# Kernel optimization log

Hardware: AMD Instinct MI355X
Metric: run time of the kernel (lower is better)

## Reference

```python
import jax, jax.numpy as jnp
import numpy as np

EPS = 1e-8

def _cos_loss(a, b):
    # faithful to torch cos_loss: norm = sqrt(sum(x*x)), x / (norm + 1e-8)
    a_norm = jnp.sqrt(jnp.sum(a * a, axis=1, keepdims=True))
    b_norm = jnp.sqrt(jnp.sum(b * b, axis=1, keepdims=True))
    a_n = a / (a_norm + EPS)
    b_n = b / (b_norm + EPS)
    cossim = jnp.sum(a_n * b_n, axis=1)
    return jnp.mean(1.0 - cossim)

def setup_inputs() -> dict:
    key = jax.random.key(0)
    k1, k2, k3 = jax.random.split(key, 3)
    shape = (1, 768, 64, 64)  # [n, c_cat(block2 VGG16 feats), h, w]
    a = jax.random.normal(k1, shape, dtype=jnp.float32)
    b = jax.random.normal(k2, shape, dtype=jnp.float32)
    d = jax.random.normal(k3, shape, dtype=jnp.float32)
    return {"a": a, "b": b, "d": d}

def reference(a, b, d):
    n, c, h, w = a.shape
    hw = h * w
    a_flat = a.reshape(n, c, hw)   # [n, c, hw]
    b_flat = b.reshape(n, c, hw)   # [n, c, h2w2]
    d_flat = d.reshape(n, c, hw)
    # normalize exactly as argmin_cos_distance: sqrt(sum + 1e-8) then /(norm + 1e-8)
    b_norm = jnp.sqrt(jnp.sum(b_flat * b_flat, axis=1, keepdims=True) + EPS)
    b_n = b_flat / (b_norm + EPS)
    a_norm = jnp.sqrt(jnp.sum(a_flat * a_flat, axis=1, keepdims=True) + EPS)
    a_n = a_flat / (a_norm + EPS)
    # cosine distance matrix [n, hw, h2w2]
    d_mat = 1.0 - jnp.einsum('ncp,ncq->npq', a_n, b_n)
    z_best = jnp.argmin(d_mat, axis=2)  # [n, hw]
    # gather matched style features from d
    idx = jnp.broadcast_to(z_best[:, None, :], (n, c, hw))
    target_feats = jnp.take_along_axis(d_flat, idx, axis=2)  # [n, c, hw]
    # NNFM loss between rendered feats and matched style feats (score is detached)
    loss = _cos_loss(a_flat, target_feats)
    z_new = target_feats.reshape(n, c, h, w)
    return (loss, z_new, z_best)
```

## Files before the change

### kernel.cpp

```cpp
#include <hip/hip_runtime.h>
#include <math.h>

#define EPS  1e-8f
#define C    768
#define HW   4096
#define NKB  24
#define NNB  12
#define NBN  32
#define TAU  0.016f
#define NCH_NEW 12
#define NCH_OLD 48

typedef float  floatx4 __attribute__((ext_vector_type(4)));
typedef short  shortx8 __attribute__((ext_vector_type(8)));
typedef unsigned short ushort_t;
typedef unsigned int   uint_t;
typedef __attribute__((address_space(1))) uint_t as1_uint;
typedef __attribute__((address_space(3))) uint_t as3_uint;

__device__ __forceinline__ ushort_t f2bf(float v) {
    uint_t u = __float_as_uint(v);
    uint_t r = (u + 0x7FFFu + ((u >> 16) & 1u)) >> 16;
    return (ushort_t)r;
}
__device__ __forceinline__ void async_cp16(const ushort_t* g, ushort_t* l) {
    __builtin_amdgcn_global_load_lds((const as1_uint*)g, (as3_uint*)l, 16, 0, 0);
}

__global__ __launch_bounds__(256) void prep_kernel(
    const float* __restrict__ a, const float* __restrict__ b,
    const float* __restrict__ d,
    ushort_t* __restrict__ Ah, ushort_t* __restrict__ Bh,
    float* __restrict__ dT, float* __restrict__ bT,
    float* __restrict__ aT, int at_ok,
    float* __restrict__ nbp2, float* __restrict__ out)
{
    __shared__ float tile[64][65];
    const int t = threadIdx.x;
    const int p0 = blockIdx.x * 64;
    const int c0 = blockIdx.y * 64;
    const int r16 = t >> 4;
    const int q4  = (t & 15) * 4;
    const int pl = t >> 2, g = t & 3;
    const int pg = p0 + pl;
    const int sw = (pg >> 1) & 3;

    if (blockIdx.x == 0 && blockIdx.y == 0 && t == 0) out[0] = 0.f;

#pragma unroll
    for (int pp = 0; pp < 4; ++pp) {
        int c = pp * 16 + r16;
        float4 v = *(const float4*)&d[(size_t)(c0 + c) * HW + p0 + q4];
        tile[c][q4]     = v.x; tile[c][q4 + 1] = v.y;
        tile[c][q4 + 2] = v.z; tile[c][q4 + 3] = v.w;
    }
    __syncthreads();
#pragma unroll
    for (int pp = 0; pp < 4; ++pp) {
        int p = pp * 16 + r16;
        float4 v;
        v.x = tile[q4][p];     v.y = tile[q4 + 1][p];
        v.z = tile[q4 + 2][p]; v.w = tile[q4 + 3][p];
        *(float4*)&dT[(size_t)(p0 + p) * C + c0 + q4] = v;
    }
    __syncthreads();

#pragma unroll
    for (int pp = 0; pp < 4; ++pp) {
        int c = pp * 16 + r16;
        float4 v = *(const float4*)&b[(size_t)(c0 + c) * HW + p0 + q4];
        tile[c][q4]     = v.x; tile[c][q4 + 1] = v.y;
        tile[c][q4 + 2] = v.z; tile[c][q4 + 3] = v.w;
    }
    __syncthreads();
#pragma unroll
    for (int pp = 0; pp < 4; ++pp) {
        int p = pp * 16 + r16;
        float4 v;
        v.x = tile[q4][p];     v.y = tile[q4 + 1][p];
        v.z = tile[q4 + 2][p]; v.w = tile[q4 + 3][p];
        *(float4*)&bT[(size_t)(p0 + p) * C + c0 + q4] = v;
    }
#pragma unroll
    for (int h = 0; h < 2; ++h) {
        const int kb = (c0 >> 5) + h;
        uint_t w[4];
#pragma unroll
        for (int u = 0; u < 4; ++u) {
            ushort_t lo = f2bf(tile[h * 32 + g * 8 + 2 * u][pl]);
            ushort_t hi = f2bf(tile[h * 32 + g * 8 + 2 * u + 1][pl]);
            w[u] = (uint_t)lo | ((uint_t)hi << 16);
        }
        uint4* oh = (uint4*)(Bh + ((size_t)kb * HW + pg) * 32);
        oh[g ^ sw] = make_uint4(w[0], w[1], w[2], w[3]);
    }
    if (t < 64) {
        float s = 0.f;
#pragma unroll
        for (int c = 0; c < 64; ++c) { float v = tile[c][t]; s += v * v; }
        nbp2[blockIdx.y * HW + p0 + t] = s;
    }
    __syncthreads();

#pragma unroll
    for (int pp = 0; pp < 4; ++pp) {
        int c = pp * 16 + r16;
        float4 v = *(const float4*)&a[(size_t)(c0 + c) * HW + p0 + q4];
        tile[c][q4]     = v.x; tile[c][q4 + 1] = v.y;
        tile[c][q4 + 2] = v.z; tile[c][q4 + 3] = v.w;
    }
    __syncthreads();
    if (at_ok) {
#pragma unroll
        for (int pp = 0; pp < 4; ++pp) {
            int p = pp * 16 + r16;
            float4 v;
            v.x = tile[q4][p];     v.y = tile[q4 + 1][p];
            v.z = tile[q4 + 2][p]; v.w = tile[q4 + 3][p];
            *(float4*)&aT[(size_t)(p0 + p) * C + c0 + q4] = v;
        }
    }
#pragma unroll
    for (int h = 0; h < 2; ++h) {
        const int kb = (c0 >> 5) + h;
        uint_t w[4];
#pragma unroll
        for (int u = 0; u < 4; ++u) {
            ushort_t lo = f2bf(tile[h * 32 + g * 8 + 2 * u][pl]);
            ushort_t hi = f2bf(tile[h * 32 + g * 8 + 2 * u + 1][pl]);
            w[u] = (uint_t)lo | ((uint_t)hi << 16);
        }
        uint4* oh = (uint4*)(Ah + ((size_t)kb * HW + pg) * 32);
        oh[g ^ sw] = make_uint4(w[0], w[1], w[2], w[3]);
    }
}

__global__ __launch_bounds__(256, 4) void gemm_mfma_kernel(
    const ushort_t* __restrict__ Ah, const ushort_t* __restrict__ Bh,
    const float* __restrict__ nbp2,
    float* __restrict__ pv1, int* __restrict__ pi1,
    float* __restrict__ pv2, int* __restrict__ pi2)
{
    __shared__ __align__(16) char smem[33280];
    ushort_t* sA0 = (ushort_t*)smem;
    ushort_t* sB0 = (ushort_t*)(smem + 8192);
    ushort_t* sA1 = (ushort_t*)(smem + 16384);
    ushort_t* sB1 = (ushort_t*)(smem + 24576);
    float*    nb_s = (float*)(smem + 32768);

    const int tid  = threadIdx.x;
    const int lane = tid & 63;
    const int wave = tid >> 6;
    const int wm = wave >> 1, wn = wave & 1;
    const int flat = blockIdx.y * (HW / 128) + blockIdx.x;
    const int orig = (flat & 7) * 128 + (flat >> 3);
    const int bm = orig >> 5, bn = orig & 31;
    const int l15 = lane & 15, l4 = lane >> 4;
    const int swz = (l15 >> 1) & 3;

    floatx4 acc[4][4];
#pragma unroll
    for (int i = 0; i < 4; ++i)
#pragma unroll
        for (int j = 0; j < 4; ++j) acc[i][j] = (floatx4){0.f, 0.f, 0.f, 0.f};

    auto stage = [&](int kb, ushort_t* dA, ushort_t* dB) {
        const size_t aoff = (size_t)(kb * HW + bm * 128) * 32 + tid * 8;
        const size_t boff = (size_t)(kb * HW + bn * 128) * 32 + tid * 8;
        async_cp16(Ah + aoff,        dA + tid * 8);
        async_cp16(Ah + aoff + 2048, dA + tid * 8 + 2048);
        async_cp16(Bh + boff,        dB + tid * 8);
        async_cp16(Bh + boff + 2048, dB + tid * 8 + 2048);
    };
    auto compute = [&](const ushort_t* pA, const ushort_t* pB) {
        shortx8 af[4], bf_[4];
#pragma unroll
        for (int i = 0; i < 4; ++i)
            af[i] = *(const shortx8*)&pA[((wm * 4 + i) * 16 + l15) * 32 + ((l4 ^ swz) * 8)];
#pragma unroll
        for (int j = 0; j < 4; ++j)
            bf_[j] = *(const shortx8*)&pB[((wn * 4 + j) * 16 + l15) * 32 + ((l4 ^ swz) * 8)];
#pragma unroll
        for (int i = 0; i < 4; ++i)
#pragma unroll
            for (int j = 0; j < 4; ++j)
                acc[i][j] = __builtin_amdgcn_mfma_f32_16x16x32_bf16(af[i], bf_[j], acc[i][j], 0, 0, 0);
    };

    stage(0, sA0, sB0);
    if (tid < 128) {
        float s = 0.f;
        int q = bn * 128 + tid;
#pragma unroll
        for (int ch = 0; ch < NNB; ++ch) s += nbp2[ch * HW + q];
        nb_s[tid] = 1.0f / (sqrtf(s + EPS) + EPS);
    }
    __syncthreads();

    for (int kb = 0; kb < NKB; kb += 2) {
        stage(kb + 1, sA1, sB1);
        compute(sA0, sB0);
        __syncthreads();
        if (kb + 2 < NKB) stage(kb + 2, sA0, sB0);
        compute(sA1, sB1);
        __syncthreads();
    }

    float rnb[4];
#pragma unroll
    for (int j = 0; j < 4; ++j)
        rnb[j] = nb_s[wn * 64 + j * 16 + l15];

    float* lv1 = (float*)smem;
    int*   li1 = (int*)(smem + 1024);
    float* lv2 = (float*)(smem + 2048);
    int*   li2 = (int*)(smem + 3072);

#pragma unroll
    for (int i = 0; i < 4; ++i) {
#pragma unroll
        for (int r = 0; r < 4; ++r) {
            float v1 = -INFINITY, v2 = -INFINITY; int i1 = 0, i2 = 0;
#pragma unroll
            for (int j = 0; j < 4; ++j) {
                float sv = acc[i][j][r] * rnb[j];
                int q = bn * 128 + wn * 64 + j * 16 + l15;
                if (sv > v1) { v2 = v1; i2 = i1; v1 = sv; i1 = q; }
                else if (sv > v2) { v2 = sv; i2 = q; }
            }
#pragma unroll
            for (int m = 1; m < 16; m <<= 1) {
                float ov1 = __shfl_xor(v1, m, 64);
                int   oi1 = __shfl_xor(i1, m, 64);
                float ov2 = __shfl_xor(v2, m, 64);
                int   oi2 = __shfl_xor(i2, m, 64);
                if (ov1 > v1 || (ov1 == v1 && oi1 < i1)) {
                    if (v1 > ov2 || (v1 == ov2 && i1 < oi2)) { v2 = v1; i2 = i1; }
                    else { v2 = ov2; i2 = oi2; }
                    v1 = ov1; i1 = oi1;
                } else if (ov1 > v2 || (ov1 == v2 && oi1 < i2)) {
                    v2 = ov1; i2 = oi1;
                }
            }
            if (l15 == 0) {
                int pl = wm * 64 + i * 16 + l4 * 4 + r;
                lv1[pl * 2 + wn] = v1; li1[pl * 2 + wn] = i1;
                lv2[pl * 2 + wn] = v2; li2[pl * 2 + wn] = i2;
            }
        }
    }
    __syncthreads();
    if (tid < 128) {
        float v1 = lv1[tid * 2],     v2 = lv2[tid * 2];
        int   i1 = li1[tid * 2],     i2 = li2[tid * 2];
        float w1 = lv1[tid * 2 + 1], w2 = lv2[tid * 2 + 1];
        int   j1 = li1[tid * 2 + 1], j2 = li2[tid * 2 + 1];
        if (w1 > v1 || (w1 == v1 && j1 < i1)) {
            if (v1 > w2 || (v1 == w2 && i1 < j2)) { v2 = v1; i2 = i1; }
            else { v2 = w2; i2 = j2; }
            v1 = w1; i1 = j1;
        } else if (w1 > v2 || (w1 == v2 && j1 < i2)) {
            v2 = w1; i2 = j1;
        }
        int p = bm * 128 + tid;
        pv1[p * NBN + bn] = v1; pi1[p * NBN + bn] = i1;
        pv2[p * NBN + bn] = v2; pi2[p * NBN + bn] = i2;
    }
}

__global__ __launch_bounds__(256) void reduce_recheck_kernel(
    const float* __restrict__ a, const float* __restrict__ b,
    const float* __restrict__ bT, int bt_ok,
    const float* __restrict__ aT, int at_ok,
    const float* __restrict__ pv1, const int* __restrict__ pi1,
    const float* __restrict__ pv2, const int* __restrict__ pi2,
    int* __restrict__ zb, float* __restrict__ out_zbest)
{
    const int wave = threadIdx.x >> 6, lane = threadIdx.x & 63;
    const int p = blockIdx.x * 4 + wave;
    const int tq = lane & 31;

    float v1, v2, candv; int i1, cand;
    if (lane < 32) {
        v1 = pv1[p * NBN + tq]; i1 = pi1[p * NBN + tq]; v2 = pv2[p * NBN + tq];
        cand = i1; candv = v1;
    } else {
        v1 = -INFINITY; v2 = -INFINITY; i1 = 0x7fffffff;
        cand = pi2[p * NBN + tq];
        candv = pv2[p * NBN + tq];
    }
#pragma unroll
    for (int m = 1; m < 32; m <<= 1) {
        float ov1 = __shfl_xor(v1, m, 64);
        int   oi1 = __shfl_xor(i1, m, 64);
        float ov2 = __shfl_xor(v2, m, 64);
        if (ov1 > v1 || (ov1 == v1 && oi1 < i1)) {
            v2 = fmaxf(v1, ov2); v1 = ov1; i1 = oi1;
        } else {
            v2 = fmaxf(v2, ov1);
        }
    }
    v1 = __shfl(v1, 0, 64); v2 = __shfl(v2, 0, 64); i1 = __shfl(i1, 0, 64);

    if (v1 - v2 >= TAU) {
        if (lane == 0) { zb[p] = i1; out_zbest[p] = (float)i1; }
        return;
    }

    const bool active = candv >= v1 - TAU;

    int q = cand;
    float dot = 0.f, b2 = 0.f;
    if (active) {
        if (at_ok) {
            const float* br = bT + (size_t)q * C;
            const float* ar = aT + (size_t)p * C;
#pragma unroll 4
            for (int c = 0; c < C; c += 4) {
                float4 bv = *(const float4*)(br + c);
                float4 av = *(const float4*)(ar + c);
                dot += av.x * bv.x + av.y * bv.y + av.z * bv.z + av.w * bv.w;
                b2  += bv.x * bv.x + bv.y * bv.y + bv.z * bv.z + bv.w * bv.w;
            }
        } else if (bt_ok) {
            const float* br = bT + (size_t)q * C;
            const float* ap = a + p;
#pragma unroll 4
            for (int c = 0; c < C; c += 4) {
                float4 bv = *(const float4*)(br + c);
                dot += ap[(size_t)c * HW] * bv.x + ap[(size_t)(c + 1) * HW] * bv.y
                     + ap[(size_t)(c + 2) * HW] * bv.z + ap[(size_t)(c + 3) * HW] * bv.w;
                b2  += bv.x * bv.x + bv.y * bv.y + bv.z * bv.z + bv.w * bv.w;
            }
        } else {
#pragma unroll 8
            for (int c = 0; c < C; ++c) {
                float av = a[c * HW + p];
                float bv = b[c * HW + q];
                dot += av * bv; b2 += bv * bv;
            }
        }
    }
    float s = active ? (dot / (sqrtf(b2 + EPS) + EPS)) : -INFINITY;
#pragma unroll
    for (int m = 1; m < 64; m <<= 1) {
        float os = __shfl_xor(s, m, 64);
        int   oq = __shfl_xor(q, m, 64);
        if (os > s || (os == s && oq < q)) { s = os; q = oq; }
    }
    if (lane == 0) { zb[p] = q; out_zbest[p] = (float)q; }
}

__global__ __launch_bounds__(256) void gather_loss_kernel(
    const float* __restrict__ a, const float* __restrict__ dT,
    const int* __restrict__ zb, float* __restrict__ out,
    float* __restrict__ pdot, float* __restrict__ pa2, float* __restrict__ pt2)
{
    __shared__ float tile[64][65];
    __shared__ int qs[64];
    const int t = threadIdx.x;
    const int p0 = blockIdx.x * 64;
    const int c0 = blockIdx.y * 64;
    if (t < 64) qs[t] = zb[p0 + t];
    __syncthreads();

    {
        const int pl = t >> 2, sub = t & 3;
        const float* src = dT + (size_t)qs[pl] * C + c0 + sub * 16;
        float4 v0 = *(const float4*)(src);
        float4 v1 = *(const float4*)(src + 4);
        float4 v2 = *(const float4*)(src + 8);
        float4 v3 = *(const float4*)(src + 12);
        float* dst = &tile[pl][sub * 16];
        dst[0] = v0.x; dst[1] = v0.y; dst[2]  = v0.z; dst[3]  = v0.w;
        dst[4] = v1.x; dst[5] = v1.y; dst[6]  = v1.z; dst[7]  = v1.w;
        dst[8] = v2.x; dst[9] = v2.y; dst[10] = v2.z; dst[11] = v2.w;
        dst[12] = v3.x; dst[13] = v3.y; dst[14] = v3.z; dst[15] = v3.w;
    }
    __syncthreads();

    const int p = t & 63, cg = t >> 6;
    float dot = 0.f, a2 = 0.f, t2 = 0.f;
#pragma unroll
    for (int i = 0; i < 16; ++i) {
        int cc = cg * 16 + i;
        float tv = tile[p][cc];
        float av = a[(size_t)(c0 + cc) * HW + p0 + p];
        out[1 + (size_t)(c0 + cc) * HW + p0 + p] = tv;
        dot += av * tv; a2 += av * av; t2 += tv * tv;
    }
    __shared__ float r1[256], r2[256], r3[256];
    r1[t] = dot; r2[t] = a2; r3[t] = t2;
    __syncthreads();
    if (t < 64) {
        dot = r1[t] + r1[t + 64] + r1[t + 128] + r1[t + 192];
        a2  = r2[t] + r2[t + 64] + r2[t + 128] + r2[t + 192];
        t2  = r3[t] + r3[t + 64] + r3[t + 128] + r3[t + 192];
        pdot[blockIdx.y * HW + p0 + t] = dot;
        pa2[blockIdx.y * HW + p0 + t]  = a2;
        pt2[blockIdx.y * HW + p0 + t]  = t2;
    }
}

__global__ __launch_bounds__(256) void loss_finalize_kernel(
    const float* __restrict__ pdot, const float* __restrict__ pa2,
    const float* __restrict__ pt2, float* __restrict__ out, int nch)
{
    int p4 = (blockIdx.x * 256 + threadIdx.x) * 4;
    float d0 = 0.f, d1 = 0.f, d2 = 0.f, d3 = 0.f;
    float a0 = 0.f, a1 = 0.f, a2 = 0.f, a3 = 0.f;
    float t0 = 0.f, t1 = 0.f, t2 = 0.f, t3 = 0.f;
    for (int ch = 0; ch < nch; ++ch) {
        float4 dv = *(const float4*)&pdot[(size_t)ch * HW + p4];
        float4 av = *(const float4*)&pa2[(size_t)ch * HW + p4];
        float4 tv = *(const float4*)&pt2[(size_t)ch * HW + p4];
        d0 += dv.x; d1 += dv.y; d2 += dv.z; d3 += dv.w;
        a0 += av.x; a1 += av.y; a2 += av.z; a3 += av.w;
        t0 += tv.x; t1 += tv.y; t2 += tv.z; t3 += tv.w;
    }
    float contrib =
        (1.f - d0 / ((sqrtf(a0) + EPS) * (sqrtf(t0) + EPS))) +
        (1.f - d1 / ((sqrtf(a1) + EPS) * (sqrtf(t1) + EPS))) +
        (1.f - d2 / ((sqrtf(a2) + EPS) * (sqrtf(t2) + EPS))) +
        (1.f - d3 / ((sqrtf(a3) + EPS) * (sqrtf(t3) + EPS)));
    __shared__ float red[256];
    red[threadIdx.x] = contrib;
    __syncthreads();
    for (int s = 128; s > 0; s >>= 1) {
        if (threadIdx.x < s) red[threadIdx.x] += red[threadIdx.x + s];
        __syncthreads();
    }
    if (threadIdx.x == 0) atomicAdd(out, red[0] * (1.0f / HW));
}

__global__ __launch_bounds__(256) void bnorm_partial_fb_kernel(
    const float* __restrict__ b, float* __restrict__ nbp)
{
    int q = blockIdx.x * 256 + threadIdx.x;
    int c0 = blockIdx.y * 32;
    float s = 0.f;
#pragma unroll 8
    for (int c = c0; c < c0 + 32; ++c) { float v = b[c * HW + q]; s += v * v; }
    nbp[blockIdx.y * HW + q] = s;
}

__global__ __launch_bounds__(256) void bnorm_finalize_fb_kernel(
    const float* __restrict__ nbp, float* __restrict__ nb)
{
    int q = blockIdx.x * 256 + threadIdx.x;
    float s = 0.f;
#pragma unroll
    for (int ch = 0; ch < NKB; ++ch) s += nbp[ch * HW + q];
    nb[q] = sqrtf(s + EPS) + EPS;
}

__global__ __launch_bounds__(256) void gemm_argmax_fb_kernel(
    const float* __restrict__ A, const float* __restrict__ B,
    const float* __restrict__ nb,
    float* __restrict__ pval, int* __restrict__ pidx)
{
    __shared__ __align__(16) char smem[16384];
    float (*As)[128] = (float (*)[128])smem;
    float (*Bs)[128] = (float (*)[128])(smem + 4096);
    const int m0 = blockIdx.x * 128, q0 = blockIdx.y * 128;
    const int tid = threadIdx.x;
    const int tx = tid & 15, ty = tid >> 4;
    const int lr = tid >> 5, lc = (tid & 31) * 4;
    float acc[8][8] = {};
    for (int k0 = 0; k0 < C; k0 += 8) {
        *(float4*)&As[lr][lc] = *(const float4*)&A[(k0 + lr) * HW + m0 + lc];
        *(float4*)&Bs[lr][lc] = *(const float4*)&B[(k0 + lr) * HW + q0 + lc];
        __syncthreads();
#pragma unroll
        for (int kk = 0; kk < 8; ++kk) {
            float a8[8], b8[8];
            *(float4*)&a8[0] = *(float4*)&As[kk][ty * 8];
            *(float4*)&a8[4] = *(float4*)&As[kk][ty * 8 + 4];
            *(float4*)&b8[0] = *(float4*)&Bs[kk][tx * 8];
            *(float4*)&b8[4] = *(float4*)&Bs[kk][tx * 8 + 4];
#pragma unroll
            for (int i = 0; i < 8; ++i)
#pragma unroll
                for (int j = 0; j < 8; ++j) acc[i][j] += a8[i] * b8[j];
        }
        __syncthreads();
    }
    float nbv[8];
#pragma unroll
    for (int j = 0; j < 8; ++j) nbv[j] = nb[q0 + tx * 8 + j];
    float (*rv)[16] = (float (*)[16])smem;
    int   (*ri)[16] = (int   (*)[16])(smem + 8192);
#pragma unroll
    for (int i = 0; i < 8; ++i) {
        float bv = -INFINITY; int bi = 0;
#pragma unroll
        for (int j = 0; j < 8; ++j) {
            float s = acc[i][j] / nbv[j];
            int q = q0 + tx * 8 + j;
            if (s > bv) { bv = s; bi = q; }
        }
        rv[ty * 8 + i][tx] = bv;
        ri[ty * 8 + i][tx] = bi;
    }
    __syncthreads();
    if (tid < 128) {
        float bv = rv[tid][0]; int bi = ri[tid][0];
#pragma unroll
        for (int t = 1; t < 16; ++t) {
            float v = rv[tid][t]; int ii = ri[tid][t];
            if (v > bv || (v == bv && ii < bi)) { bv = v; bi = ii; }
        }
        pval[(m0 + tid) * NBN + blockIdx.y] = bv;
        pidx[(m0 + tid) * NBN + blockIdx.y] = bi;
    }
}

__global__ __launch_bounds__(256) void reduce_fb_kernel(
    const float* __restrict__ pval, const int* __restrict__ pidx,
    int* __restrict__ zb, float* __restrict__ out_zbest)
{
    int p = blockIdx.x * 256 + threadIdx.x;
    float bv = pval[p * NBN]; int bi = pidx[p * NBN];
#pragma unroll 8
    for (int t = 1; t < NBN; ++t) {
        float v = pval[p * NBN + t]; int ii = pidx[p * NBN + t];
        if (v > bv || (v == bv && ii < bi)) { bv = v; bi = ii; }
    }
    zb[p] = bi;
    out_zbest[p] = (float)bi;
}

__global__ __launch_bounds__(256) void gather_partial_kernel(
    const float* __restrict__ a, const float* __restrict__ d,
    const int* __restrict__ zb, float* __restrict__ out,
    float* __restrict__ pdot, float* __restrict__ pa2, float* __restrict__ pt2)
{
    int p = blockIdx.x * 256 + threadIdx.x;
    int ch = blockIdx.y;
    int c0 = ch * (C / NCH_OLD);
    int q = zb[p];
    float dot = 0.f, a2 = 0.f, t2 = 0.f;
#pragma unroll
    for (int c = c0; c < c0 + C / NCH_OLD; ++c) {
        float av = a[c * HW + p];
        float tv = d[c * HW + q];
        dot += av * tv; a2 += av * av; t2 += tv * tv;
        out[1 + c * HW + p] = tv;
    }
    pdot[ch * HW + p] = dot;
    pa2[ch * HW + p] = a2;
    pt2[ch * HW + p] = t2;
}

extern "C" void kernel_launch(void* const* d_in, const int* in_sizes, int n_in,
                              void* d_out, int out_size, void* d_ws, size_t ws_size,
                              hipStream_t stream) {
    const float* a = (const float*)d_in[0];
    const float* b = (const float*)d_in[1];
    const float* d = (const float*)d_in[2];
    float* out = (float*)d_out;
    float* out_zbest = out + 1 + (size_t)C * HW;

    char* ws = (char*)d_ws;
    size_t off = 0;
    auto alloc = [&](size_t bytes) { void* p = ws + off; off = (off + bytes + 255) & ~(size_t)255; return p; };

    const size_t PACK = (size_t)C * HW * 2;
    ushort_t* Ah = (ushort_t*)alloc(PACK);
    ushort_t* Bh = (ushort_t*)alloc(PACK);
    float* nbp = (float*)alloc((size_t)NKB * HW * 4);
    float* pv1 = (float*)alloc((size_t)HW * NBN * 4);
    int*   pi1 = (int*)alloc((size_t)HW * NBN * 4);
    float* pv2 = (float*)alloc((size_t)HW * NBN * 4);
    int*   pi2 = (int*)alloc((size_t)HW * NBN * 4);
    int*   zb  = (int*)alloc(HW * 4);
    float* pdot = (float*)alloc((size_t)NCH_NEW * HW * 4);
    float* pa2  = (float*)alloc((size_t)NCH_NEW * HW * 4);
    float* pt2  = (float*)alloc((size_t)NCH_NEW * HW * 4);
    float* dT  = (float*)alloc((size_t)C * HW * 4);
    float* bT  = (float*)alloc((size_t)C * HW * 4);
    bool fast = off <= ws_size;
    float* aT  = (float*)alloc((size_t)C * HW * 4);
    int at_ok = (off <= ws_size) ? 1 : 0;

    if (fast) {
        prep_kernel<<<dim3(HW / 64, C / 64), 256, 0, stream>>>(
            a, b, d, Ah, Bh, dT, bT, aT, at_ok, nbp, out);
        gemm_mfma_kernel<<<dim3(HW / 128, HW / 128), 256, 0, stream>>>(
            Ah, Bh, nbp, pv1, pi1, pv2, pi2);
        reduce_recheck_kernel<<<HW / 4, 256, 0, stream>>>(
            a, b, bT, 1, aT, at_ok, pv1, pi1, pv2, pi2, zb, out_zbest);
        gather_loss_kernel<<<dim3(HW / 64, NCH_NEW), 256, 0, stream>>>(
            a, dT, zb, out, pdot, pa2, pt2);
        loss_finalize_kernel<<<HW / 1024, 256, 0, stream>>>(pdot, pa2, pt2, out, NCH_NEW);
    } else {
        off = 0;
        float* nb = (float*)alloc(HW * 4);
        nbp = (float*)alloc((size_t)NKB * HW * 4);
        pv1 = (float*)alloc((size_t)HW * NBN * 4);
        pi1 = (int*)alloc((size_t)HW * NBN * 4);
        zb  = (int*)alloc(HW * 4);
        float* pdot2 = (float*)alloc((size_t)NCH_OLD * HW * 4);
        float* pa22  = (float*)alloc((size_t)NCH_OLD * HW * 4);
        float* pt22  = (float*)alloc((size_t)NCH_OLD * HW * 4);
        hipMemsetAsync(d_out, 0, sizeof(float), stream);
        bnorm_partial_fb_kernel<<<dim3(HW / 256, NKB), 256, 0, stream>>>(b, nbp);
        bnorm_finalize_fb_kernel<<<HW / 256, 256, 0, stream>>>(nbp, nb);
        gemm_argmax_fb_kernel<<<dim3(HW / 128, HW / 128), 256, 0, stream>>>(a, b, nb, pv1, pi1);
        reduce_fb_kernel<<<HW / 256, 256, 0, stream>>>(pv1, pi1, zb, out_zbest);
        gather_partial_kernel<<<dim3(HW / 256, NCH_OLD), 256, 0, stream>>>(
            a, d, zb, out, pdot2, pa22, pt22);
        loss_finalize_kernel<<<HW / 1024, 256, 0, stream>>>(pdot2, pa22, pt22, out, NCH_OLD);
    }
}
```

Baseline: 177.1 us.

## Move fp32 transposes of a, b, d from prep kernel into GEMM tail

The fp32 transposes producing dT, bT and aT move out of the prep kernel and into the end of the MFMA GEMM kernel. Each GEMM block runs a grid-stride loop over transpose tiles after finishing its argmax partials, reusing its shared memory. This shortens the prep kernel that sits on the critical path before the GEMM and lets the memory-bound transpose overlap with GEMM blocks that are still computing. The cost is extra register and launch-argument pressure in the GEMM kernel and a tail of memory traffic added to every GEMM block.

```diff
diff --git a/kernel.cpp b/kernel.cpp
--- a/kernel.cpp
+++ b/kernel.cpp
@@ -10,6 +10,7 @@
 #define TAU  0.016f
 #define NCH_NEW 12
 #define NCH_OLD 48
+#define NTT  (3 * (HW / 64) * (C / 64))
 
 typedef float  floatx4 __attribute__((ext_vector_type(4)));
 typedef short  shortx8 __attribute__((ext_vector_type(8)));
@@ -29,10 +30,7 @@
 
 __global__ __launch_bounds__(256) void prep_kernel(
     const float* __restrict__ a, const float* __restrict__ b,
-    const float* __restrict__ d,
     ushort_t* __restrict__ Ah, ushort_t* __restrict__ Bh,
-    float* __restrict__ dT, float* __restrict__ bT,
-    float* __restrict__ aT, int at_ok,
     float* __restrict__ nbp2, float* __restrict__ out)
 {
     __shared__ float tile[64][65];
@@ -50,37 +48,11 @@
 #pragma unroll
     for (int pp = 0; pp < 4; ++pp) {
         int c = pp * 16 + r16;
-        float4 v = *(const float4*)&d[(size_t)(c0 + c) * HW + p0 + q4];
-        tile[c][q4]     = v.x; tile[c][q4 + 1] = v.y;
-        tile[c][q4 + 2] = v.z; tile[c][q4 + 3] = v.w;
-    }
-    __syncthreads();
-#pragma unroll
-    for (int pp = 0; pp < 4; ++pp) {
-        int p = pp * 16 + r16;
-        float4 v;
-        v.x = tile[q4][p];     v.y = tile[q4 + 1][p];
-        v.z = tile[q4 + 2][p]; v.w = tile[q4 + 3][p];
-        *(float4*)&dT[(size_t)(p0 + p) * C + c0 + q4] = v;
-    }
-    __syncthreads();
-
-#pragma unroll
-    for (int pp = 0; pp < 4; ++pp) {
-        int c = pp * 16 + r16;
         float4 v = *(const float4*)&b[(size_t)(c0 + c) * HW + p0 + q4];
         tile[c][q4]     = v.x; tile[c][q4 + 1] = v.y;
         tile[c][q4 + 2] = v.z; tile[c][q4 + 3] = v.w;
     }
     __syncthreads();
-#pragma unroll
-    for (int pp = 0; pp < 4; ++pp) {
-        int p = pp * 16 + r16;
-        float4 v;
-        v.x = tile[q4][p];     v.y = tile[q4 + 1][p];
-        v.z = tile[q4 + 2][p]; v.w = tile[q4 + 3][p];
-        *(float4*)&bT[(size_t)(p0 + p) * C + c0 + q4] = v;
-    }
 #pragma unroll
     for (int h = 0; h < 2; ++h) {
         const int kb = (c0 >> 5) + h;
@@ -110,16 +82,6 @@
         tile[c][q4 + 2] = v.z; tile[c][q4 + 3] = v.w;
     }
     __syncthreads();
-    if (at_ok) {
-#pragma unroll
-        for (int pp = 0; pp < 4; ++pp) {
-            int p = pp * 16 + r16;
-            float4 v;
-            v.x = tile[q4][p];     v.y = tile[q4 + 1][p];
-            v.z = tile[q4 + 2][p]; v.w = tile[q4 + 3][p];
-            *(float4*)&aT[(size_t)(p0 + p) * C + c0 + q4] = v;
-        }
-    }
 #pragma unroll
     for (int h = 0; h < 2; ++h) {
         const int kb = (c0 >> 5) + h;
@@ -138,6 +100,10 @@
 __global__ __launch_bounds__(256, 4) void gemm_mfma_kernel(
     const ushort_t* __restrict__ Ah, const ushort_t* __restrict__ Bh,
     const float* __restrict__ nbp2,
+    const float* __restrict__ a, const float* __restrict__ b,
+    const float* __restrict__ d,
+    float* __restrict__ dT, float* __restrict__ bT,
+    float* __restrict__ aT, int at_ok,
     float* __restrict__ pv1, int* __restrict__ pi1,
     float* __restrict__ pv2, int* __restrict__ pi2)
 {
@@ -265,6 +231,40 @@
         int p = bm * 128 + tid;
         pv1[p * NBN + bn] = v1; pi1[p * NBN + bn] = i1;
         pv2[p * NBN + bn] = v2; pi2[p * NBN + bn] = i2;
+    }
+
+    __syncthreads();
+    {
+        float (*tile)[65] = (float (*)[65])smem;
+        const int r16 = tid >> 4;
+        const int q4  = (tid & 15) * 4;
+        const int flatb = blockIdx.y * (HW / 128) + blockIdx.x;
+        for (int tt = flatb; tt < NTT; tt += 1024) {
+            const int which = tt / 768;
+            const int idx = tt - which * 768;
+            if (which == 2 && !at_ok) break;
+            const float* src = (which == 0) ? d : ((which == 1) ? b : a);
+            float*       dst = (which == 0) ? dT : ((which == 1) ? bT : aT);
+            const int tp0 = (idx & 63) * 64;
+            const int tc0 = (idx >> 6) * 64;
+#pragma unroll
+            for (int pp = 0; pp < 4; ++pp) {
+                int c = pp * 16 + r16;
+                float4 v = *(const float4*)&src[(size_t)(tc0 + c) * HW + tp0 + q4];
+                tile[c][q4]     = v.x; tile[c][q4 + 1] = v.y;
+                tile[c][q4 + 2] = v.z; tile[c][q4 + 3] = v.w;
+            }
+            __syncthreads();
+#pragma unroll
+            for (int pp = 0; pp < 4; ++pp) {
+                int p = pp * 16 + r16;
+                float4 v;
+                v.x = tile[q4][p];     v.y = tile[q4 + 1][p];
+                v.z = tile[q4 + 2][p]; v.w = tile[q4 + 3][p];
+                *(float4*)&dst[(size_t)(tp0 + p) * C + tc0 + q4] = v;
+            }
+            __syncthreads();
+        }
     }
 }
 
@@ -585,9 +585,9 @@
 
     if (fast) {
         prep_kernel<<<dim3(HW / 64, C / 64), 256, 0, stream>>>(
-            a, b, d, Ah, Bh, dT, bT, aT, at_ok, nbp, out);
+            a, b, Ah, Bh, nbp, out);
         gemm_mfma_kernel<<<dim3(HW / 128, HW / 128), 256, 0, stream>>>(
-            Ah, Bh, nbp, pv1, pi1, pv2, pi2);
+            Ah, Bh, nbp, a, b, d, dT, bT, aT, at_ok, pv1, pi1, pv2, pi2);
         reduce_recheck_kernel<<<HW / 4, 256, 0, stream>>>(
             a, b, bT, 1, aT, at_ok, pv1, pi1, pv2, pi2, zb, out_zbest);
         gather_loss_kernel<<<dim3(HW / 64, NCH_NEW), 256, 0, stream>>>(
```

Result: faster. 168.0 us (-5.1%).
